# Performance work log

Measured on AMD Instinct MI355X. Metric: run time of the kernel, lower is better.

The kernel has to match this reference:

```python
import jax, jax.numpy as jnp
import numpy as np

DIM = 2048
N_HEADS = 16
N_KV_HEADS = 8
HEAD_DIM = DIM // N_HEADS  # 128
N_REP = N_HEADS // N_KV_HEADS  # 2
HIDDEN = 4 * DIM  # Project hidden dim
SEQ = 2048
BSZ = 2
ROPE_THETA = 10000.0
NEG_INF = -1e9


def setup_inputs() -> dict:
    key = jax.random.key(0)
    ks = jax.random.split(key, 10)
    s_in = 1.0 / np.sqrt(DIM)
    s_hid = 1.0 / np.sqrt(HIDDEN)
    x = jax.random.normal(ks[0], (BSZ, SEQ, DIM), jnp.float32)
    wq = jax.random.normal(ks[1], (DIM, N_HEADS * HEAD_DIM), jnp.float32) * s_in
    wk_w1 = jax.random.normal(ks[2], (DIM, HIDDEN), jnp.float32) * s_in
    wk_w2 = jax.random.normal(ks[3], (HIDDEN, N_KV_HEADS * HEAD_DIM), jnp.float32) * s_hid
    wk_w3 = jax.random.normal(ks[4], (DIM, HIDDEN), jnp.float32) * s_in
    wv_w1 = jax.random.normal(ks[5], (DIM, HIDDEN), jnp.float32) * s_in
    wv_w2 = jax.random.normal(ks[6], (HIDDEN, N_KV_HEADS * HEAD_DIM), jnp.float32) * s_hid
    wv_w3 = jax.random.normal(ks[7], (DIM, HIDDEN), jnp.float32) * s_in
    wo = jax.random.normal(ks[8], (N_HEADS * HEAD_DIM, DIM), jnp.float32) * s_in
    # RoPE tables: angle[t, j] = t * theta^(-2j/head_dim), j in [0, head_dim/2)
    inv_freq = 1.0 / (ROPE_THETA ** (np.arange(0, HEAD_DIM, 2, dtype=np.float64) / HEAD_DIM))
    ang = np.outer(np.arange(SEQ, dtype=np.float64), inv_freq)
    freqs_cos = jnp.asarray(np.cos(ang), jnp.float32)  # [SEQ, HEAD_DIM//2]
    freqs_sin = jnp.asarray(np.sin(ang), jnp.float32)
    # causal additive mask [1, 1, SEQ, SEQ]
    mask = jnp.triu(jnp.full((SEQ, SEQ), NEG_INF, jnp.float32), k=1)[None, None]
    return {
        "x": x, "wq": wq,
        "wk_w1": wk_w1, "wk_w2": wk_w2, "wk_w3": wk_w3,
        "wv_w1": wv_w1, "wv_w2": wv_w2, "wv_w3": wv_w3,
        "wo": wo, "freqs_cos": freqs_cos, "freqs_sin": freqs_sin,
        "mask": mask, "start_pos": 0,
    }


def _rope(x, cos, sin):
    # x: [b, s, h, d]; pairs (x[2j], x[2j+1]) rotated as complex multiply
    xr = x[..., 0::2]
    xi = x[..., 1::2]
    c = cos[None, :, None, :]
    s = sin[None, :, None, :]
    out_r = xr * c - xi * s
    out_i = xr * s + xi * c
    return jnp.stack([out_r, out_i], axis=-1).reshape(x.shape)


def _project(x, w1, w2, w3):
    # SwiGLU-style projection: w2(silu(x@w1) * (x@w3))
    return (jax.nn.silu(x @ w1) * (x @ w3)) @ w2


def reference(x, wq, wk_w1, wk_w2, wk_w3, wv_w1, wv_w2, wv_w3, wo,
              freqs_cos, freqs_sin, mask, start_pos):
    b, s, _ = x.shape
    q = (x @ wq).reshape(b, s, N_HEADS, HEAD_DIM)
    q = _rope(q, freqs_cos, freqs_sin)
    k = _project(x, wk_w1, wk_w2, wk_w3).reshape(b, s, N_KV_HEADS, HEAD_DIM)
    v = _project(x, wv_w1, wv_w2, wv_w3).reshape(b, s, N_KV_HEADS, HEAD_DIM)
    k = _rope(k, freqs_cos, freqs_sin)
    o_keys, o_values = k, v  # is_training=True path: cache is just current k/v
    # repeat_kv (GQA) -> [b, h, s, d]
    kr = jnp.repeat(k, N_REP, axis=2).transpose(0, 2, 1, 3)
    vr = jnp.repeat(v, N_REP, axis=2).transpose(0, 2, 1, 3)
    qt = q.transpose(0, 2, 1, 3)
    scores = jnp.einsum('bhqd,bhkd->bhqk', qt, kr) / np.sqrt(HEAD_DIM).astype(np.float32)
    scores = scores + mask
    attn = jax.nn.softmax(scores.astype(jnp.float32), axis=-1).astype(qt.dtype)
    out = jnp.einsum('bhqk,bhkd->bhqd', attn, vr)
    out = out.transpose(0, 2, 1, 3).reshape(b, s, N_HEADS * HEAD_DIM)
    return (out @ wo, o_keys, o_values)
```

## Files before the change

kernel.cpp:

```cpp
#include <hip/hip_runtime.h>

typedef unsigned short ushort_t;
typedef __attribute__((ext_vector_type(4))) float f32x4;
typedef __attribute__((ext_vector_type(8))) __bf16 bf16x8;
typedef __attribute__((ext_vector_type(4))) unsigned short ushort4_t;
typedef __attribute__((ext_vector_type(8))) unsigned short ushort8_t;
typedef __attribute__((ext_vector_type(2))) unsigned int u32x2;

#define AS1 __attribute__((address_space(1)))
#define AS3 __attribute__((address_space(3)))

__device__ __forceinline__ float bf2f(ushort_t u) {
  unsigned int v = ((unsigned int)u) << 16;
  return __builtin_bit_cast(float, v);
}
__device__ __forceinline__ ushort_t f2bf(float f) {
  unsigned int u = __builtin_bit_cast(unsigned int, f);
  u += 0x7fffu + ((u >> 16) & 1u);
  return (ushort_t)(u >> 16);
}
__device__ __forceinline__ void storeC(float* p, float v) { *p = v; }
__device__ __forceinline__ void storeC(ushort_t* p, float v) { *p = f2bf(v); }

__global__ __launch_bounds__(256) void cast_f32_bf16(const float* __restrict__ in,
                                                     ushort_t* __restrict__ outp) {
  size_t i = ((size_t)blockIdx.x * 256 + threadIdx.x) * 4;
  f32x4 v = *(const f32x4*)(const void*)&in[i];
  ushort4_t o;
#pragma unroll
  for (int j = 0; j < 4; ++j) o[j] = f2bf(v[j]);
  *(ushort4_t*)(void*)&outp[i] = o;
}

__global__ __launch_bounds__(256) void transpose_cast_b(
    const float* __restrict__ W0, const float* __restrict__ W1,
    const float* __restrict__ W2, const float* __restrict__ W3,
    ushort_t* __restrict__ Wt, int K, int N, long long strT) {
  __shared__ float tile[32][33];
  const int z = blockIdx.z;
  const float* W = (z == 0) ? W0 : (z == 1) ? W1 : (z == 2) ? W2 : W3;
  ushort_t* out = Wt + (size_t)(strT * z);
  int n0 = blockIdx.x * 32, k0 = blockIdx.y * 32;
  int tx = threadIdx.x, ty = threadIdx.y;
#pragma unroll
  for (int i = 0; i < 4; ++i)
    tile[ty + 8 * i][tx] = W[(size_t)(k0 + ty + 8 * i) * N + n0 + tx];
  __syncthreads();
#pragma unroll
  for (int i = 0; i < 4; ++i)
    out[(size_t)(n0 + ty + 8 * i) * K + k0 + tx] = f2bf(tile[tx][ty + 8 * i]);
}

__global__ __launch_bounds__(256) void transpose_cast_glu(
    const float* __restrict__ W1k, const float* __restrict__ W3k,
    const float* __restrict__ W1v, const float* __restrict__ W3v,
    ushort_t* __restrict__ out, long long strT) {
  __shared__ float tile[32][33];
  const int z = blockIdx.z;
  const float* W = (z == 0) ? W1k : (z == 1) ? W3k : (z == 2) ? W1v : W3v;
  ushort_t* o = out + (size_t)((z >> 1) * strT);
  const int zz = z & 1;
  int n0 = blockIdx.x * 32, k0 = blockIdx.y * 32;
  int tx = threadIdx.x, ty = threadIdx.y;
#pragma unroll
  for (int i = 0; i < 4; ++i)
    tile[ty + 8 * i][tx] = W[(size_t)(k0 + ty + 8 * i) * 8192 + n0 + tx];
  __syncthreads();
#pragma unroll
  for (int i = 0; i < 4; ++i) {
    int n = n0 + ty + 8 * i;
    int br = ((n >> 4) * 32) + zz * 16 + (n & 15);
    o[(size_t)br * 2048 + k0 + tx] = f2bf(tile[tx][ty + 8 * i]);
  }
}

__global__ __launch_bounds__(256) void reduce_q(const ushort_t* __restrict__ part,
                                                ushort_t* __restrict__ qb,
                                                const float* __restrict__ fc,
                                                const float* __restrict__ fs) {
  const float alpha = 0.08838834764831845f;
  int p = blockIdx.x * 256 + threadIdx.x;
  size_t e0 = (size_t)p * 8;
  int i0 = (int)((e0 & 127) >> 1);
  int s = (int)((e0 >> 11) & 2047);
  ushort8_t a = *(const ushort8_t*)(const void*)&part[e0];
  ushort8_t b = *(const ushort8_t*)(const void*)&part[e0 + 8388608];
  f32x4 c4 = *(const f32x4*)(const void*)&fc[s * 64 + i0];
  f32x4 s4 = *(const f32x4*)(const void*)&fs[s * 64 + i0];
  ushort8_t o;
#pragma unroll
  for (int j = 0; j < 4; ++j) {
    float xr = bf2f(a[2 * j]) + bf2f(b[2 * j]);
    float xi = bf2f(a[2 * j + 1]) + bf2f(b[2 * j + 1]);
    float c = c4[j] * alpha, sn = s4[j] * alpha;
    o[2 * j] = f2bf(xr * c - xi * sn);
    o[2 * j + 1] = f2bf(xr * sn + xi * c);
  }
  *(ushort8_t*)(void*)&qb[e0] = o;
}

__global__ __launch_bounds__(256) void reduce_k(const ushort_t* __restrict__ part,
                                                ushort_t* __restrict__ kb,
                                                float* __restrict__ okeys,
                                                const float* __restrict__ fc,
                                                const float* __restrict__ fs) {
  int p = blockIdx.x * 256 + threadIdx.x;
  size_t e0 = (size_t)p * 8;
  int i0 = (int)((e0 & 127) >> 1);
  int s = (int)((e0 >> 10) & 2047);
  ushort8_t a0 = *(const ushort8_t*)(const void*)&part[e0];
  ushort8_t a1 = *(const ushort8_t*)(const void*)&part[e0 + 4194304];
  ushort8_t a2 = *(const ushort8_t*)(const void*)&part[e0 + 8388608];
  ushort8_t a3 = *(const ushort8_t*)(const void*)&part[e0 + 12582912];
  f32x4 c4 = *(const f32x4*)(const void*)&fc[s * 64 + i0];
  f32x4 s4 = *(const f32x4*)(const void*)&fs[s * 64 + i0];
  ushort8_t o;
  f32x4 ov0, ov1;
#pragma unroll
  for (int j = 0; j < 4; ++j) {
    float xr = bf2f(a0[2 * j]) + bf2f(a1[2 * j]) + bf2f(a2[2 * j]) + bf2f(a3[2 * j]);
    float xi = bf2f(a0[2 * j + 1]) + bf2f(a1[2 * j + 1]) + bf2f(a2[2 * j + 1]) +
               bf2f(a3[2 * j + 1]);
    float c = c4[j], sn = s4[j];
    float orr = xr * c - xi * sn;
    float oi = xr * sn + xi * c;
    o[2 * j] = f2bf(orr);
    o[2 * j + 1] = f2bf(oi);
    if (j < 2) { ov0[2 * j] = orr; ov0[2 * j + 1] = oi; }
    else       { ov1[2 * (j - 2)] = orr; ov1[2 * (j - 2) + 1] = oi; }
  }
  *(ushort8_t*)(void*)&kb[e0] = o;
  *(f32x4*)(void*)&okeys[e0] = ov0;
  *(f32x4*)(void*)&okeys[e0 + 4] = ov1;
}

__global__ __launch_bounds__(256) void reduce_v(const ushort_t* __restrict__ part,
                                                float* __restrict__ ovals,
                                                ushort_t* __restrict__ vbT) {
  __shared__ ushort_t tile[32][33];
  int s0 = blockIdx.x * 32, d0 = blockIdx.y * 32, bk = blockIdx.z;
  int b = bk >> 3, kh = bk & 7;
  int tx = threadIdx.x, ty = threadIdx.y;
#pragma unroll
  for (int i = 0; i < 4; ++i) {
    int s = s0 + ty + 8 * i;
    size_t src = ((size_t)(b * 2048 + s)) * 1024 + kh * 128 + d0 + tx;
    float v = bf2f(part[src]) + bf2f(part[src + 4194304]) +
              bf2f(part[src + 8388608]) + bf2f(part[src + 12582912]);
    tile[ty + 8 * i][tx] = f2bf(v);
    ovals[src] = v;
  }
  __syncthreads();
#pragma unroll
  for (int i = 0; i < 4; ++i) {
    int d = d0 + ty + 8 * i;
    vbT[((size_t)bk * 128 + d) * 2048 + s0 + tx] = tile[tx][ty + 8 * i];
  }
}

__global__ __launch_bounds__(256) void reduce_wo(const ushort_t* __restrict__ part,
                                                 float* __restrict__ outp) {
  size_t e0 = ((size_t)blockIdx.x * 256 + threadIdx.x) * 8;
  ushort8_t a = *(const ushort8_t*)(const void*)&part[e0];
  ushort8_t b = *(const ushort8_t*)(const void*)&part[e0 + 8388608];
  f32x4 o0, o1;
#pragma unroll
  for (int j = 0; j < 4; ++j) {
    o0[j] = bf2f(a[j]) + bf2f(b[j]);
    o1[j] = bf2f(a[j + 4]) + bf2f(b[j + 4]);
  }
  *(f32x4*)(void*)&outp[e0] = o0;
  *(f32x4*)(void*)&outp[e0 + 4] = o1;
}

__global__ __launch_bounds__(256) void flash_attn(
    const ushort_t* __restrict__ Q, const ushort_t* __restrict__ Kg,
    const ushort_t* __restrict__ VT, ushort_t* __restrict__ O) {
  __shared__ __align__(16) char smem[81920];
  const int xq = blockIdx.x;
  const int bh = blockIdx.y;
  const int qi = (bh & 16) ? (15 - xq) : xq;
  const int b = bh >> 4, h = bh & 15, kh = h >> 1;
  const int t = threadIdx.x, w = t >> 6, lane = t & 63;
  const int fr = lane & 15, fh = lane >> 4;
  const size_t kelem0 = ((size_t)b * 2048) * 1024 + kh * 128;
  const size_t velem0 = ((size_t)(b * 8 + kh)) * 128 * 2048;
  const size_t qrow0 = (size_t)b * 2048;

  size_t oK[4], oV[4];
#pragma unroll
  for (int qv = 0; qv < 4; ++qv) {
    int row = w * 16 + qv * 4 + (lane >> 4);
    oK[qv] = (size_t)row * 1024 + (((lane & 15) ^ (row & 7)) * 8);
    int rd = w * 32 + qv * 8 + (lane >> 3);
    oV[qv] = (size_t)rd * 2048 + (((lane & 7) ^ (rd & 7)) * 8);
  }

  auto stage = [&](int tile, int buf) {
    const size_t kc = (size_t)tile * 64 * 1024;
    const int vc = tile * 64;
    char* kd = smem + buf * 16384 + w * 4096;
    char* vd = smem + 32768 + buf * 16384 + w * 4096;
#pragma unroll
    for (int qv = 0; qv < 4; ++qv) {
      __builtin_amdgcn_global_load_lds((const AS1 void*)(Kg + kelem0 + kc + oK[qv]),
                                       (AS3 void*)(kd + qv * 1024), 16, 0, 0);
      __builtin_amdgcn_global_load_lds((const AS1 void*)(VT + velem0 + oV[qv] + vc),
                                       (AS3 void*)(vd + qv * 1024), 16, 0, 0);
    }
  };

  const int qw = qi * 128 + w * 32;
  const int nt = 2 * qi + 2;

  bf16x8 qF[2][4];
#pragma unroll
  for (int qt = 0; qt < 2; ++qt)
#pragma unroll
    for (int i = 0; i < 4; ++i)
      qF[qt][i] = *(const bf16x8*)(const void*)(
          Q + (qrow0 + qw + qt * 16 + fr) * 2048 + h * 128 + i * 32 + fh * 8);

  f32x4 acco[8][2] = {};
  float mrun[2] = {-1e30f, -1e30f};
  float lrun[2] = {0.0f, 0.0f};

  stage(0, 0);
#pragma unroll 1
  for (int tt = 0; tt < nt; ++tt) {
    const int c0 = tt * 64;
    if (tt + 1 < nt) {
      stage(tt + 1, (tt + 1) & 1);
      asm volatile("s_waitcnt vmcnt(8)" ::: "memory");
    } else {
      asm volatile("s_waitcnt vmcnt(0)" ::: "memory");
    }
    __builtin_amdgcn_sched_barrier(0);
    __builtin_amdgcn_s_barrier();
    const char* KL = smem + (tt & 1) * 16384;
    const char* VL = smem + 32768 + (tt & 1) * 16384;
    char* PL = smem + 65536 + w * 4096;
    if (c0 <= qw + 31) {
      f32x4 sacc[2][4] = {};
#pragma unroll
      for (int i = 0; i < 4; ++i)
#pragma unroll
        for (int mt = 0; mt < 4; ++mt) {
          bf16x8 kf = *(const bf16x8*)(const void*)(
              KL + (mt * 16 + fr) * 256 + (((i * 4 + fh) ^ (fr & 7)) * 16));
          sacc[0][mt] = __builtin_amdgcn_mfma_f32_16x16x32_bf16(kf, qF[0][i], sacc[0][mt], 0, 0, 0);
          sacc[1][mt] = __builtin_amdgcn_mfma_f32_16x16x32_bf16(kf, qF[1][i], sacc[1][mt], 0, 0, 0);
        }
      if (c0 + 63 > qw) {
#pragma unroll
        for (int qt = 0; qt < 2; ++qt) {
          int qg = qw + qt * 16 + fr;
#pragma unroll
          for (int mt = 0; mt < 4; ++mt)
#pragma unroll
            for (int j = 0; j < 4; ++j)
              if (c0 + mt * 16 + fh * 4 + j > qg) sacc[qt][mt][j] = -1e30f;
        }
      }
#pragma unroll
      for (int qt = 0; qt < 2; ++qt) {
        float mt_ = -1e30f;
#pragma unroll
        for (int mt = 0; mt < 4; ++mt)
#pragma unroll
          for (int j = 0; j < 4; ++j) mt_ = fmaxf(mt_, sacc[qt][mt][j]);
        mt_ = fmaxf(mt_, __shfl_xor(mt_, 16, 64));
        mt_ = fmaxf(mt_, __shfl_xor(mt_, 32, 64));
        float mnew = fmaxf(mrun[qt], mt_);
        float corr = __expf(mrun[qt] - mnew);
        mrun[qt] = mnew;
        float ps = 0.0f;
        float pv[4][4];
#pragma unroll
        for (int mt = 0; mt < 4; ++mt)
#pragma unroll
          for (int j = 0; j < 4; ++j) {
            float pe = __expf(sacc[qt][mt][j] - mnew);
            pv[mt][j] = pe;
            ps += pe;
          }
        ps += __shfl_xor(ps, 16, 64);
        ps += __shfl_xor(ps, 32, 64);
        lrun[qt] = lrun[qt] * corr + ps;
#pragma unroll
        for (int mt = 0; mt < 4; ++mt) {
          unsigned int u0, u1;
          asm("v_cvt_pk_bf16_f32 %0, %1, %2" : "=v"(u0) : "v"(pv[mt][0]), "v"(pv[mt][1]));
          asm("v_cvt_pk_bf16_f32 %0, %1, %2" : "=v"(u1) : "v"(pv[mt][2]), "v"(pv[mt][3]));
          u32x2 val;
          val[0] = u0;
          val[1] = u1;
          *(u32x2*)(void*)(PL + qt * 2048 + fr * 128 +
                           (((2 * mt + (fh >> 1)) ^ (fr & 7)) * 16) + (fh & 1) * 8) = val;
        }
#pragma unroll
        for (int dt = 0; dt < 8; ++dt) acco[dt][qt] *= corr;
      }
      bf16x8 pf[2][2];
#pragma unroll
      for (int qt = 0; qt < 2; ++qt)
#pragma unroll
        for (int ks = 0; ks < 2; ++ks)
          pf[qt][ks] = *(const bf16x8*)(const void*)(
              PL + qt * 2048 + fr * 128 + (((ks * 4 + fh) ^ (fr & 7)) * 16));
#pragma unroll
      for (int dt = 0; dt < 8; ++dt)
#pragma unroll
        for (int ks = 0; ks < 2; ++ks) {
          bf16x8 vf = *(const bf16x8*)(const void*)(
              VL + (dt * 16 + fr) * 128 + (((ks * 4 + fh) ^ (fr & 7)) * 16));
          acco[dt][0] = __builtin_amdgcn_mfma_f32_16x16x32_bf16(vf, pf[0][ks], acco[dt][0], 0, 0, 0);
          acco[dt][1] = __builtin_amdgcn_mfma_f32_16x16x32_bf16(vf, pf[1][ks], acco[dt][1], 0, 0, 0);
        }
    }
    __builtin_amdgcn_s_barrier();
  }
#pragma unroll
  for (int qt = 0; qt < 2; ++qt) {
    float inv = 1.0f / lrun[qt];
    const size_t rb = (qrow0 + qw + qt * 16 + fr) * 2048 + h * 128;
#pragma unroll
    for (int dt = 0; dt < 8; ++dt) {
      ushort4_t o4;
#pragma unroll
      for (int j = 0; j < 4; ++j) o4[j] = f2bf(acco[dt][qt][j] * inv);
      *(ushort4_t*)(void*)(O + rb + dt * 16 + fh * 4) = o4;
    }
  }
}

#define GEMM_PHASE(ABUF, BBUF, Q, STAGE_STMT, TAIL_STMT)                        \
  {                                                                             \
    if ((Q) == 0) {                                                             \
      _Pragma("unroll") for (int nf = 0; nf < 4; ++nf) {                        \
        const char* bp = (BBUF) + ((wn * 64 + nf * 16 + fr) << 7);              \
        bF[nf][0] = *(const bf16x8*)(const void*)(bp + sl);                     \
        bF[nf][1] = *(const bf16x8*)(const void*)(bp + (sl ^ 64));              \
      }                                                                         \
    }                                                                           \
    _Pragma("unroll") for (int mi = 0; mi < 2; ++mi) {                          \
      const char* ap = (ABUF) + ((wm * 128 + ((Q)*2 + mi) * 16 + fr) << 7);     \
      aF[mi][0] = *(const bf16x8*)(const void*)(ap + sl);                       \
      aF[mi][1] = *(const bf16x8*)(const void*)(ap + (sl ^ 64));                \
    }                                                                           \
    STAGE_STMT;                                                                 \
    if ((Q) == 0) asm volatile("s_waitcnt lgkmcnt(8)" ::: "memory");            \
    __builtin_amdgcn_s_barrier();                                               \
    asm volatile("s_waitcnt lgkmcnt(0)" ::: "memory");                          \
    __builtin_amdgcn_sched_barrier(0);                                          \
    __builtin_amdgcn_s_setprio(1);                                              \
    _Pragma("unroll") for (int mi = 0; mi < 2; ++mi)                            \
      _Pragma("unroll") for (int nf = 0; nf < 4; ++nf) {                        \
        acc[(Q)*2 + mi][nf] = __builtin_amdgcn_mfma_f32_16x16x32_bf16(          \
            aF[mi][0], bF[nf][0], acc[(Q)*2 + mi][nf], 0, 0, 0);                \
        acc[(Q)*2 + mi][nf] = __builtin_amdgcn_mfma_f32_16x16x32_bf16(          \
            aF[mi][1], bF[nf][1], acc[(Q)*2 + mi][nf], 0, 0, 0);                \
      }                                                                         \
    __builtin_amdgcn_s_setprio(0);                                              \
    TAIL_STMT;                                                                  \
    __builtin_amdgcn_sched_barrier(0);                                          \
    __builtin_amdgcn_s_barrier();                                               \
  }

#define GEMM_BODY                                                               \
  f32x4 acc[8][4] = {};                                                         \
  const int NT = K >> 6;                                                        \
  const int NI = NT >> 1;                                                       \
  char* const A0 = (char*)smem;                                                 \
  char* const A1 = (char*)smem + 32768;                                         \
  char* const B0 = (char*)smem + 65536;                                         \
  char* const B1 = (char*)smem + 98304;                                         \
         \
  auto stageA = [&](int tile, int h) {                                          \
    char* base = (char*)smem + ((tile & 1) << 15);                              \
    const ushort_t* src = gA + tile * 64 + (size_t)(h * 64) * lda;              \
    __builtin_amdgcn_global_load_lds((const AS1 void*)src,                      \
        (AS3 void*)(base + h * 8192 + w * 1024), 16, 0, 0);                     \
    __builtin_amdgcn_global_load_lds(                                           \
        (const AS1 void*)(src + (size_t)128 * lda),                             \
        (AS3 void*)(base + 16384 + h * 8192 + w * 1024), 16, 0, 0);             \
  };                                                                            \
  auto stageB = [&](int tile, int h) {                                          \
    char* base = (char*)smem + 65536 + ((tile & 1) << 15);                      \
    const ushort_t* src = gB + tile * 64 + (size_t)(h * 128) * ldb;             \
    __builtin_amdgcn_global_load_lds((const AS1 void*)src,                      \
        (AS3 void*)(base + h * 16384 + w * 1024), 16, 0, 0);                    \
    __builtin_amdgcn_global_load_lds(                                           \
        (const AS1 void*)(src + (size_t)64 * ldb),                              \
        (AS3 void*)(base + h * 16384 + 8192 + w * 1024), 16, 0, 0);             \
  };                                                                            \
     \
  stageB(0, 0); stageB(0, 1); stageA(0, 0); stageA(0, 1);                       \
  stageB(1, 0); stageB(1, 1); stageA(1, 0);                                     \
  asm volatile("s_waitcnt vmcnt(6)" ::: "memory");                              \
  __builtin_amdgcn_sched_barrier(0);                                            \
  __builtin_amdgcn_s_barrier();                                                 \
  __builtin_amdgcn_sched_barrier(0);                                            \
  for (int i = 0; i < NI; ++i) {                                                \
    const int T1 = 2 * i + 1, T2 = 2 * i + 2, T3 = 2 * i + 3;                   \
    const bool s2 = T2 < NT, s3 = T3 < NT;                                      \
    bf16x8 bF[4][2], aF[2][2];                                                  \
                                            \
    GEMM_PHASE(A0, B0, 0, { stageA(T1, 1); }, {})                               \
    GEMM_PHASE(A0, B0, 1, { if (s2) stageB(T2, 0); }, {})                       \
    GEMM_PHASE(A0, B0, 2, { if (s2) stageB(T2, 1); }, {})                       \
    GEMM_PHASE(A0, B0, 3, { if (s2) stageA(T2, 0); },                           \
               { if (s2) asm volatile("s_waitcnt vmcnt(6)" ::: "memory");       \
                 else    asm volatile("s_waitcnt vmcnt(0)" ::: "memory"); })    \
                                          \
    GEMM_PHASE(A1, B1, 0, { if (s2) stageA(T2, 1); }, {})                       \
    GEMM_PHASE(A1, B1, 1, { if (s3) stageB(T3, 0); }, {})                       \
    GEMM_PHASE(A1, B1, 2, { if (s3) stageB(T3, 1); }, {})                       \
    GEMM_PHASE(A1, B1, 3, { if (s3) stageA(T3, 0); },                           \
               { if (s2) asm volatile("s_waitcnt vmcnt(6)" ::: "memory"); })    \
  }

template <typename CT>
__global__ __launch_bounds__(512, 2) void gemm256(
    const ushort_t* __restrict__ A, const ushort_t* __restrict__ B,
    CT* __restrict__ C, int K, int lda, int ldb, int ldc,
    int nwgx, int nwg, long long strA, long long strB, long long strC) {
  __shared__ __align__(16) char smem[131072];
  const int bz = blockIdx.y;
  const int bid = blockIdx.x;
  const int swz = (bid & 7) * (nwg >> 3) + (bid >> 3);
  const int r0 = (swz / nwgx) * 256;
  const int c0 = (swz % nwgx) * 256;
  const int t = threadIdx.x, w = t >> 6, lane = t & 63;
  const int wm = w >> 2, wn = w & 3;
  const int fr = lane & 15, fh = lane >> 4;
  const int sl = (fh ^ (fr & 7)) << 4;
  const int srow = t >> 3;
  const int scb = (t & 7) ^ (srow & 7);
  const ushort_t* gA = A + strA * bz + (size_t)(r0 + srow) * lda + scb * 8;
  const ushort_t* gB = B + strB * bz + (size_t)(c0 + srow) * ldb + scb * 8;

  GEMM_BODY

  CT* gC = C + strC * bz;
  const int cr = r0 + wm * 128 + fh * 4;
  const int cc = c0 + wn * 64 + fr;
#pragma unroll
  for (int m = 0; m < 8; ++m)
#pragma unroll
    for (int n = 0; n < 4; ++n)
#pragma unroll
      for (int j = 0; j < 4; ++j)
        storeC(&gC[(size_t)(cr + m * 16 + j) * ldc + cc + n * 16], acc[m][n][j]);
}

__global__ __launch_bounds__(512, 2) void gemm256_glu(
    const ushort_t* __restrict__ A, const ushort_t* __restrict__ B,
    ushort_t* __restrict__ C, int K, int lda, int ldb, int ldc,
    int nwgx, int nwg) {
  __shared__ __align__(16) char smem[131072];
  const int bid = blockIdx.x;
  const int swz = (bid & 7) * (nwg >> 3) + (bid >> 3);
  const int r0 = (swz / nwgx) * 256;
  const int c0 = (swz % nwgx) * 256;
  const int t = threadIdx.x, w = t >> 6, lane = t & 63;
  const int wm = w >> 2, wn = w & 3;
  const int fr = lane & 15, fh = lane >> 4;
  const int sl = (fh ^ (fr & 7)) << 4;
  const int srow = t >> 3;
  const int scb = (t & 7) ^ (srow & 7);
  const ushort_t* gA = A + (size_t)(r0 + srow) * lda + scb * 8;
  const ushort_t* gB = B + (size_t)(c0 + srow) * ldb + scb * 8;

  GEMM_BODY

  const int cr = r0 + wm * 128 + fh * 4;
  const int cc2 = (c0 >> 1) + wn * 32 + fr;
#pragma unroll
  for (int m = 0; m < 8; ++m)
#pragma unroll
    for (int pp = 0; pp < 2; ++pp)
#pragma unroll
      for (int j = 0; j < 4; ++j) {
        float g1 = acc[m][2 * pp][j];
        float g3 = acc[m][2 * pp + 1][j];
        float hv = g1 / (1.0f + __expf(-g1)) * g3;
        C[(size_t)(cr + m * 16 + j) * ldc + cc2 + pp * 16] = f2bf(hv);
      }
}

extern "C" void kernel_launch(void* const* d_in, const int* in_sizes, int n_in,
                              void* d_out, int out_size, void* d_ws, size_t ws_size,
                              hipStream_t stream) {
  const float* x = (const float*)d_in[0];
  const float* wq = (const float*)d_in[1];
  const float* wk1 = (const float*)d_in[2];
  const float* wk2 = (const float*)d_in[3];
  const float* wk3 = (const float*)d_in[4];
  const float* wv1 = (const float*)d_in[5];
  const float* wv2 = (const float*)d_in[6];
  const float* wv3 = (const float*)d_in[7];
  const float* wo = (const float*)d_in[8];
  const float* fc = (const float*)d_in[9];
  const float* fs = (const float*)d_in[10];

  float* outp = (float*)d_out;
  float* okeys = outp + 8388608;
  float* ovals = outp + 12582912;

  char* p = (char*)d_ws;
  auto alloc = [&](size_t bytes) {
    char* r = p;
    p += (bytes + 255) & ~(size_t)255;
    return r;
  };
  ushort_t* xb = (ushort_t*)alloc(8388608ull * 2);
  ushort_t* w4T = (ushort_t*)alloc(4ull * 16777216 * 2);
  ushort_t* w2T = (ushort_t*)alloc(2ull * 8388608 * 2);
  ushort_t* wqoT = (ushort_t*)alloc(2ull * 4194304 * 2);
  ushort_t* qb = (ushort_t*)alloc(8388608ull * 2);
  ushort_t* kb = (ushort_t*)alloc(4194304ull * 2);
  ushort_t* vbT = (ushort_t*)alloc(4194304ull * 2);
  ushort_t* ob = (ushort_t*)alloc(8388608ull * 2);
  char* hreg = alloc(134217728ull);
  ushort_t* hbuf = (ushort_t*)hreg;
  ushort_t* partQ16 = (ushort_t*)hreg;
  ushort_t* partWO16 = (ushort_t*)hreg;
  ushort_t* part16 = (ushort_t*)w4T;

  ushort_t* Bk = w4T;
  ushort_t* Bv = w4T + 2ull * 16777216;
  ushort_t* wk2T = w2T;
  ushort_t* wv2T = w2T + 8388608;
  ushort_t* wqT = wqoT;
  ushort_t* woT = wqoT + 4194304;

  dim3 tb(32, 8);

  cast_f32_bf16<<<8192, 256, 0, stream>>>(x, xb);
  transpose_cast_glu<<<dim3(256, 64, 4), tb, 0, stream>>>(wk1, wk3, wv1, wv3,
                                                          w4T, 33554432);
  transpose_cast_b<<<dim3(32, 256, 2), tb, 0, stream>>>(wk2, wv2, wk2, wv2, w2T,
                                                        8192, 1024, 8388608);
  transpose_cast_b<<<dim3(64, 64, 2), tb, 0, stream>>>(wq, wo, wq, wo, wqoT,
                                                       2048, 2048, 4194304);

  gemm256<ushort_t><<<dim3(128, 2), 512, 0, stream>>>(
      xb, wqT, partQ16, 1024, 2048, 2048, 2048, 8, 128, 1024, 1024, 8388608);
  reduce_q<<<4096, 256, 0, stream>>>(partQ16, qb, fc, fs);

  gemm256_glu<<<dim3(1024, 1), 512, 0, stream>>>(
      xb, Bk, hbuf, 2048, 2048, 2048, 8192, 64, 1024);
  gemm256<ushort_t><<<dim3(64, 4), 512, 0, stream>>>(
      hbuf, wk2T, part16, 2048, 8192, 8192, 1024, 4, 64, 2048, 2048, 4194304);
  reduce_k<<<2048, 256, 0, stream>>>(part16, kb, okeys, fc, fs);

  gemm256_glu<<<dim3(1024, 1), 512, 0, stream>>>(
      xb, Bv, hbuf, 2048, 2048, 2048, 8192, 64, 1024);
  gemm256<ushort_t><<<dim3(64, 4), 512, 0, stream>>>(
      hbuf, wv2T, part16, 2048, 8192, 8192, 1024, 4, 64, 2048, 2048, 4194304);
  reduce_v<<<dim3(64, 4, 16), tb, 0, stream>>>(part16, ovals, vbT);

  flash_attn<<<dim3(16, 32), 256, 0, stream>>>(qb, kb, vbT, ob);

  gemm256<ushort_t><<<dim3(128, 2), 512, 0, stream>>>(
      ob, woT, partWO16, 1024, 2048, 2048, 2048, 8, 128, 1024, 1024, 8388608);
  reduce_wo<<<4096, 256, 0, stream>>>(partWO16, outp);

  (void)in_sizes; (void)n_in; (void)out_size; (void)ws_size;
}
```

Measured before the change: 933.7 us.

## Replace GLU GEMM main loop with register-double-buffered single-barrier pipeline

```diff
diff --git a/kernel.cpp b/kernel.cpp
--- a/kernel.cpp
+++ b/kernel.cpp
@@ -367,7 +367,7 @@
     __builtin_amdgcn_s_barrier();                                               \
   }
 
-#define GEMM_BODY                                                               \
+#define GEMM_BODY_PH                                                            \
   f32x4 acc[8][4] = {};                                                         \
   const int NT = K >> 6;                                                        \
   const int NI = NT >> 1;                                                       \
@@ -375,7 +375,6 @@
   char* const A1 = (char*)smem + 32768;                                         \
   char* const B0 = (char*)smem + 65536;                                         \
   char* const B1 = (char*)smem + 98304;                                         \
-         \
   auto stageA = [&](int tile, int h) {                                          \
     char* base = (char*)smem + ((tile & 1) << 15);                              \
     const ushort_t* src = gA + tile * 64 + (size_t)(h * 64) * lda;              \
@@ -394,7 +393,6 @@
         (const AS1 void*)(src + (size_t)64 * ldb),                              \
         (AS3 void*)(base + h * 16384 + 8192 + w * 1024), 16, 0, 0);             \
   };                                                                            \
-     \
   stageB(0, 0); stageB(0, 1); stageA(0, 0); stageA(0, 1);                       \
   stageB(1, 0); stageB(1, 1); stageA(1, 0);                                     \
   asm volatile("s_waitcnt vmcnt(6)" ::: "memory");                              \
@@ -405,14 +403,12 @@
     const int T1 = 2 * i + 1, T2 = 2 * i + 2, T3 = 2 * i + 3;                   \
     const bool s2 = T2 < NT, s3 = T3 < NT;                                      \
     bf16x8 bF[4][2], aF[2][2];                                                  \
-                                            \
     GEMM_PHASE(A0, B0, 0, { stageA(T1, 1); }, {})                               \
     GEMM_PHASE(A0, B0, 1, { if (s2) stageB(T2, 0); }, {})                       \
     GEMM_PHASE(A0, B0, 2, { if (s2) stageB(T2, 1); }, {})                       \
     GEMM_PHASE(A0, B0, 3, { if (s2) stageA(T2, 0); },                           \
                { if (s2) asm volatile("s_waitcnt vmcnt(6)" ::: "memory");       \
                  else    asm volatile("s_waitcnt vmcnt(0)" ::: "memory"); })    \
-                                          \
     GEMM_PHASE(A1, B1, 0, { if (s2) stageA(T2, 1); }, {})                       \
     GEMM_PHASE(A1, B1, 1, { if (s3) stageB(T3, 0); }, {})                       \
     GEMM_PHASE(A1, B1, 2, { if (s3) stageB(T3, 1); }, {})                       \
@@ -440,7 +436,7 @@
   const ushort_t* gA = A + strA * bz + (size_t)(r0 + srow) * lda + scb * 8;
   const ushort_t* gB = B + strB * bz + (size_t)(c0 + srow) * ldb + scb * 8;
 
-  GEMM_BODY
+  GEMM_BODY_PH
 
   CT* gC = C + strC * bz;
   const int cr = r0 + wm * 128 + fh * 4;
@@ -467,12 +463,117 @@
   const int wm = w >> 2, wn = w & 3;
   const int fr = lane & 15, fh = lane >> 4;
   const int sl = (fh ^ (fr & 7)) << 4;
+  const int ldsw = w * 1024;
   const int srow = t >> 3;
   const int scb = (t & 7) ^ (srow & 7);
+  const int NT = K >> 6;
   const ushort_t* gA = A + (size_t)(r0 + srow) * lda + scb * 8;
   const ushort_t* gB = B + (size_t)(c0 + srow) * ldb + scb * 8;
 
-  GEMM_BODY
+  auto stage = [&](int tile, int isB, int h) {
+    const ushort_t* g = isB ? gB : gA;
+    const size_t ld = isB ? (size_t)ldb : (size_t)lda;
+    char* lp = (char*)smem + (isB ? 65536 : 0) + ((tile & 1) << 15) + (h << 14) + ldsw;
+    const ushort_t* src = g + (size_t)(h * 128) * ld + tile * 64;
+    __builtin_amdgcn_global_load_lds((const AS1 void*)src, (AS3 void*)lp, 16, 0, 0);
+    __builtin_amdgcn_global_load_lds((const AS1 void*)(src + 64 * ld),
+                                     (AS3 void*)(lp + 8192), 16, 0, 0);
+  };
+
+  f32x4 acc[8][4] = {};
+
+  stage(0, 0, 0); stage(0, 1, 0); stage(0, 0, 1); stage(0, 1, 1);
+  asm volatile("s_waitcnt vmcnt(0)" ::: "memory");
+  __builtin_amdgcn_sched_barrier(0);
+  __builtin_amdgcn_s_barrier();
+  __builtin_amdgcn_sched_barrier(0);
+
+  const int aBase = wm * 16384 + fr * 128;
+  const int bBase = 65536 + wn * 8192 + fr * 128;
+
+  bf16x8 aX[4], aY[4], bX[4], bY[4];
+  {
+    const char* la0 = (const char*)smem + aBase;
+    const char* lb0 = (const char*)smem + bBase;
+#pragma unroll
+    for (int m = 0; m < 4; ++m)
+      aX[m] = *(const bf16x8*)(const void*)(la0 + m * 2048 + sl);
+#pragma unroll
+    for (int n = 0; n < 4; ++n)
+      bX[n] = *(const bf16x8*)(const void*)(lb0 + n * 2048 + sl);
+  }
+
+  for (int kt = 0; kt < NT; ++kt) {
+    const int buf = (kt & 1) << 15;
+    const char* la = (const char*)smem + buf + aBase;
+    const char* lb = (const char*)smem + buf + bBase;
+#pragma unroll
+    for (int m = 0; m < 4; ++m)
+      aY[m] = *(const bf16x8*)(const void*)(la + (m + 4) * 2048 + sl);
+    __builtin_amdgcn_sched_barrier(0);
+    __builtin_amdgcn_s_setprio(1);
+#pragma unroll
+    for (int m = 0; m < 4; ++m)
+#pragma unroll
+      for (int n = 0; n < 4; ++n)
+        acc[m][n] = __builtin_amdgcn_mfma_f32_16x16x32_bf16(aX[m], bX[n], acc[m][n], 0, 0, 0);
+    __builtin_amdgcn_s_setprio(0);
+    __builtin_amdgcn_sched_barrier(0);
+#pragma unroll
+    for (int m = 0; m < 4; ++m)
+      aX[m] = *(const bf16x8*)(const void*)(la + m * 2048 + (sl ^ 64));
+#pragma unroll
+    for (int n = 0; n < 4; ++n)
+      bY[n] = *(const bf16x8*)(const void*)(lb + n * 2048 + (sl ^ 64));
+    if (kt + 1 < NT) {
+      stage(kt + 1, 0, 0); stage(kt + 1, 1, 0);
+      stage(kt + 1, 0, 1); stage(kt + 1, 1, 1);
+    }
+    __builtin_amdgcn_sched_barrier(0);
+    __builtin_amdgcn_s_setprio(1);
+#pragma unroll
+    for (int m = 0; m < 4; ++m)
+#pragma unroll
+      for (int n = 0; n < 4; ++n)
+        acc[m + 4][n] = __builtin_amdgcn_mfma_f32_16x16x32_bf16(aY[m], bX[n], acc[m + 4][n], 0, 0, 0);
+    __builtin_amdgcn_s_setprio(0);
+    __builtin_amdgcn_sched_barrier(0);
+#pragma unroll
+    for (int m = 0; m < 4; ++m)
+      aY[m] = *(const bf16x8*)(const void*)(la + (m + 4) * 2048 + (sl ^ 64));
+    __builtin_amdgcn_sched_barrier(0);
+    __builtin_amdgcn_s_setprio(1);
+#pragma unroll
+    for (int m = 0; m < 4; ++m)
+#pragma unroll
+      for (int n = 0; n < 4; ++n)
+        acc[m][n] = __builtin_amdgcn_mfma_f32_16x16x32_bf16(aX[m], bY[n], acc[m][n], 0, 0, 0);
+    __builtin_amdgcn_s_setprio(0);
+    __builtin_amdgcn_sched_barrier(0);
+    __builtin_amdgcn_s_setprio(1);
+#pragma unroll
+    for (int m = 0; m < 4; ++m)
+#pragma unroll
+      for (int n = 0; n < 4; ++n)
+        acc[m + 4][n] = __builtin_amdgcn_mfma_f32_16x16x32_bf16(aY[m], bY[n], acc[m + 4][n], 0, 0, 0);
+    __builtin_amdgcn_s_setprio(0);
+    if (kt + 1 < NT) {
+      asm volatile("s_waitcnt vmcnt(0)" ::: "memory");
+      __builtin_amdgcn_sched_barrier(0);
+      __builtin_amdgcn_s_barrier();
+      __builtin_amdgcn_sched_barrier(0);
+      const int nbuf = ((kt + 1) & 1) << 15;
+      const char* lan = (const char*)smem + nbuf + aBase;
+      const char* lbn = (const char*)smem + nbuf + bBase;
+#pragma unroll
+      for (int m = 0; m < 4; ++m)
+        aX[m] = *(const bf16x8*)(const void*)(lan + m * 2048 + sl);
+#pragma unroll
+      for (int n = 0; n < 4; ++n)
+        bX[n] = *(const bf16x8*)(const void*)(lbn + n * 2048 + sl);
+      __builtin_amdgcn_sched_barrier(0);
+    }
+  }
 
   const int cr = r0 + wm * 128 + fh * 4;
   const int cc2 = (c0 >> 1) + wn * 32 + fr;
```

After: 942.0 us. Within noise of the previous version (+0.9%).
